# Performance work log

Measured on AMD Instinct MI355X. Metric: run time of the kernel, lower is better.

The kernel has to match this reference:

```python
import jax, jax.numpy as jnp
import numpy as np
from jax import lax

# 2D MPS-RNN (one-site, hilbert_local=2, real params, snake order, 'regular' phase)
# Faithful reconstruction of MPS_RNN_2D forward: site-by-site recurrence over an
# L x M lattice. At each site: candidate hidden states for both local occupations
#   h_cand[s] = M_h[i,j,s] @ h_left + M_v[i,j,s] @ h_below + v[i,j,s]
# conditional prob p(s) ~ sum_d eta[i,j,d]^2 * h_cand[s,d]^2 (eta-weighted norm),
# selected hidden state is renormalized; phase accumulates arg(w.h + c) (0 or pi
# for real params). Returns [B,2]: (log|psi|, phase).

L, M, S, D = 8, 8, 2, 32   # rows, cols, local Hilbert dim, bond dim dcut
B = 32768                  # batch of sampled configurations
NQ = L * M                 # nqubits
EPS = 1e-10


def setup_inputs() -> dict:
    key = jax.random.key(0)
    ks = jax.random.split(key, 7)
    sc = np.float32(1.0 / np.sqrt(D))  # keep hidden-state norms O(1)
    x = jax.random.randint(ks[0], (B, NQ), 0, 2, dtype=jnp.int32)
    M_h = jax.random.normal(ks[1], (L, M, S, D, D), jnp.float32) * sc
    M_v = jax.random.normal(ks[2], (L, M, S, D, D), jnp.float32) * sc
    v = jax.random.normal(ks[3], (L, M, S, D), jnp.float32) * sc
    w = jax.random.normal(ks[4], (L, M, D), jnp.float32) * sc
    c = jnp.zeros((L, M), jnp.float32)
    eta = jax.random.normal(ks[5], (L, M, D), jnp.float32)
    return {"x": x, "M_h": M_h, "M_v": M_v, "v": v, "w": w, "c": c, "eta": eta}


def _forward(x, M_h, M_v, v, w, c, eta):
    dt = M_h.dtype
    # snake order: odd rows are scanned right-to-left in lattice coordinates.
    cols = jnp.arange(M)
    odd = (jnp.arange(L) % 2 == 1)[:, None]
    colmap = jnp.where(odd, M - 1 - cols[None, :], cols[None, :])  # [L,M] scan-pos -> lattice col (involution)
    ri = jnp.arange(L)[:, None]
    gather = lambda p: p[ri, colmap]  # reorder params into scan order per row
    M_h_s, M_v_s, v_s, w_s, c_s, eta_s = (gather(p) for p in (M_h, M_v, v, w, c, eta))
    x_s = x.reshape(B, L, M).transpose(1, 2, 0)  # [L,M,B] already in qubit/scan order

    pi_f = jnp.asarray(np.pi, dt)

    def col_step(h_h, cin):
        Mh, Mv, vv, ww, cc, ee, xx, hv = cin
        # candidate states for both local occupations: [B,S,D]
        hc = (jnp.einsum('sab,Bb->Bsa', Mh, h_h)
              + jnp.einsum('sab,Bb->Bsa', Mv, hv)
              + vv[None])
        p = jnp.einsum('Bsa,a->Bs', hc * hc, ee * ee)  # eta-weighted squared norms
        psel = jnp.take_along_axis(p, xx[:, None], axis=1)[:, 0]
        dla = 0.5 * (jnp.log(psel + EPS) - jnp.log(p.sum(-1) + EPS))
        hsel = jnp.take_along_axis(hc, xx[:, None, None], axis=1)[:, 0]  # [B,D]
        hn = hsel / (jnp.sqrt(jnp.sum(hsel * hsel, -1, keepdims=True)) + EPS)
        a = hn @ ww + cc  # [B]
        dph = jnp.where(a < 0, pi_f, jnp.asarray(0, dt))  # arg of real scalar
        return hn, (dla, dph, hn)

    def row_step(carry, rin):
        h_v_lat, la, ph = carry
        Mh_r, Mv_r, v_r, w_r, c_r, e_r, x_r, cmap = rin
        hv_scan = h_v_lat[:, cmap].transpose(1, 0, 2)  # [M,B,D] vertical inputs in scan order
        h0 = jnp.ones((B, D), dt)  # left_boundary = ones
        _, (dlas, dphs, hs) = lax.scan(col_step, h0, (Mh_r, Mv_r, v_r, w_r, c_r, e_r, x_r, hv_scan))
        la = la + dlas.sum(0)
        ph = ph + dphs.sum(0)
        h_new = hs.transpose(1, 0, 2)[:, cmap]  # back to lattice column order (cmap is an involution)
        return (h_new, la, ph), None

    init = (jnp.zeros((B, M, D), dt),  # bottom_boundary = zeros
            jnp.zeros((B,), dt), jnp.zeros((B,), dt))
    (hv, log_amp, phase), _ = lax.scan(row_step, init, (M_h_s, M_v_s, v_s, w_s, c_s, eta_s, x_s, colmap))
    return jnp.stack([log_amp, phase], axis=-1)  # [B,2]


def reference(x, M_h, M_v, v, w, c, eta):
    return _forward(x, M_h, M_v, v, w, c, eta)
```

## Files before the change

kernel.cpp:

```cpp
#include <hip/hip_runtime.h>

#define LROWS 8
#define MCOLS 8
#define BD 32
#define NSITE 64
#define SPB 64
#define BTOT 32768
#define NBLK (BTOT / SPB)
#define EPS 1e-10
#define PI_D 3.14159265358979323846

#define W_OFF 0
#define CB_OFF 262144
#define CC_OFF (262144 + 12288)
#define WS_DBLS (CC_OFF + 64)

__global__ void precompute_kernel(const float* __restrict__ M_h,
                                  const float* __restrict__ M_v,
                                  const float* __restrict__ v,
                                  const float* __restrict__ w,
                                  const float* __restrict__ cc,
                                  const float* __restrict__ eta,
                                  double* __restrict__ ws) {
    int idx = blockIdx.x * 256 + threadIdx.x;
    if (idx >= WS_DBLS) return;
    double val = 0.0;
    if (idx < CB_OFF) {
        int pair = idx & 1, a8 = (idx >> 1) & 7, b = (idx >> 4) & 31;
        int r = (idx >> 9) & 7, site = idx >> 12;
        int i = site >> 3, js = site & 7;
        int c = (i & 1) ? (MCOLS - 1 - js) : js;
        int s = r >> 2, a = (r & 3) * 8 + a8;
        if (pair == 0) val = (double)M_h[(((i * MCOLS + c) * 2 + s) * BD + a) * BD + b];
        else           val = (double)M_v[(((i * MCOLS + c) * 2 + s) * BD + a) * BD + b];
    } else if (idx < CC_OFF) {
        int j = idx - CB_OFF;
        int site = j / 192;
        int rem = j - site * 192;
        int r = rem / 24, t = rem - r * 24;
        int i = site >> 3, js = site & 7;
        int c = (i & 1) ? (MCOLS - 1 - js) : js;
        int s = r >> 2, a0 = (r & 3) * 8;
        if (t < 8)       val = (double)v[(((i * MCOLS + c) * 2 + s) * BD) + a0 + t];
        else if (t < 16) { double e = (double)eta[(i * MCOLS + c) * BD + a0 + (t - 8)]; val = e * e; }
        else             val = (double)w[(i * MCOLS + c) * BD + a0 + (t - 16)];
    } else {
        int site = idx - CC_OFF;
        int i = site >> 3, js = site & 7;
        int c = (i & 1) ? (MCOLS - 1 - js) : js;
        val = (double)cc[i * MCOLS + c];
    }
    ws[idx] = val;
}

__launch_bounds__(512, 2)
__global__ void mps_main_kernel(const int* __restrict__ x,
                                const double* __restrict__ ws,
                                float* __restrict__ out) {
    __shared__ double hRow[MCOLS][BD][SPB];
    __shared__ double hOnes[BD][SPB];
    __shared__ double pbuf[8][SPB];
    __shared__ double ssb[8][SPB];
    __shared__ double phb[8][SPB];

    const int tid = threadIdx.x;
    const int k = tid & 63;
    const int r = tid >> 6;
    const int r_u = __builtin_amdgcn_readfirstlane(r);
    const int s = r_u >> 2;
    const int abase = (r_u & 3) * 8;
    const long kg = (long)blockIdx.x * SPB + k;

    for (int t = tid; t < MCOLS * BD * SPB; t += 512) (&hRow[0][0][0])[t] = 0.0;
    for (int t = tid; t < BD * SPB; t += 512) (&hOnes[0][0])[t] = 1.0;
    __syncthreads();

    const double2* __restrict__ Wp = (const double2*)ws;

    double la = 0.0, ph = 0.0;
    double2 wreg[2][16];

    {
        const double2* __restrict__ w0 = Wp + (size_t)(0 * 8 + r_u) * 256;
        #pragma unroll
        for (int t = 0; t < 16; ++t) wreg[0][t] = w0[t];
    }

    for (int i = 0; i < LROWS; ++i) {
        const int* xp = x + kg * NSITE + i * MCOLS;
        int4 xa = *reinterpret_cast<const int4*>(xp);
        int4 xb = *reinterpret_cast<const int4*>(xp + 4);
        const unsigned xbits = (unsigned)((xa.x & 1)        | ((xa.y & 1) << 1) |
                                          ((xa.z & 1) << 2) | ((xa.w & 1) << 3) |
                                          ((xb.x & 1) << 4) | ((xb.y & 1) << 5) |
                                          ((xb.z & 1) << 6) | ((xb.w & 1) << 7));
        double prodN = 1.0, prodD = 1.0;

        for (int js = 0; js < MCOLS; ++js) {
            const int site = i * MCOLS + js;
            const int c = (i & 1) ? (MCOLS - 1 - js) : js;
            const int cprev = (i & 1) ? (MCOLS - js) : (js - 1);

            const double2* __restrict__ wsite = Wp + (size_t)(site * 8 + r_u) * 256;
            const double*  __restrict__ cb    = ws + CB_OFF + (size_t)(site * 8 + r_u) * 24;

            const double* __restrict__ colV = &hRow[c][0][0];
            const double* __restrict__ colL = (js == 0) ? &hOnes[0][0] : &hRow[cprev][0][0];

            double acc[8];
            #pragma unroll
            for (int a = 0; a < 8; ++a) acc[a] = 0.0;

            #pragma unroll
            for (int bb = 0; bb < 16; ++bb) {
                const int cur = bb & 1;
                if (bb < 15) {
                    const double2* __restrict__ wn = wsite + (bb + 1) * 16;
                    #pragma unroll
                    for (int t = 0; t < 16; ++t) wreg[cur ^ 1][t] = wn[t];
                }
                #pragma unroll
                for (int bq = 0; bq < 2; ++bq) {
                    const int b = bb * 2 + bq;
                    const double hlb = colL[b * SPB + k];
                    const double hvb = colV[b * SPB + k];
                    #pragma unroll
                    for (int a = 0; a < 8; ++a) {
                        const double2 w2 = wreg[cur][bq * 8 + a];
                        acc[a] = fma(w2.x, hlb, fma(w2.y, hvb, acc[a]));
                    }
                }
            }
            #pragma unroll
            for (int a = 0; a < 8; ++a) acc[a] += cb[a];

            double pp = 0.0, ssp = 0.0, php = 0.0;
            #pragma unroll
            for (int a = 0; a < 8; ++a) {
                const double t2 = acc[a] * acc[a];
                pp  = fma(t2, cb[8 + a], pp);
                ssp += t2;
                php = fma(acc[a], cb[16 + a], php);
            }
            const double ccoef = ws[CC_OFF + site];
            const int xs = (int)((xbits >> js) & 1u);
            const bool sel = (s == xs);

            pbuf[r][k] = pp;
            ssb[r][k]  = ssp;
            phb[r][k]  = php;
            __syncthreads();

            {
                const double2* __restrict__ wn = Wp + (size_t)((site + 1) * 8 + r_u) * 256;
                #pragma unroll
                for (int t = 0; t < 16; ++t) wreg[0][t] = wn[t];
            }

            const double p0 = ((pbuf[0][k] + pbuf[1][k]) + pbuf[2][k]) + pbuf[3][k];
            const double p1 = ((pbuf[4][k] + pbuf[5][k]) + pbuf[6][k]) + pbuf[7][k];
            const double psel = xs ? p1 : p0;
            prodN *= (psel + EPS);
            prodD *= (p0 + p1 + EPS);

            const int gb = xs * 4;
            const double ss = ((ssb[gb][k] + ssb[gb + 1][k]) + ssb[gb + 2][k]) + ssb[gb + 3][k];
            const double inv = 1.0 / (sqrt(ss) + EPS);
            if (sel) {
                #pragma unroll
                for (int a = 0; a < 8; ++a)
                    hRow[c][abase + a][k] = acc[a] * inv;
            }
            const double phd = ((phb[gb][k] + phb[gb + 1][k]) + phb[gb + 2][k]) + phb[gb + 3][k];
            const double aph = phd * inv + ccoef;
            ph += (aph < 0.0) ? PI_D : 0.0;

            __syncthreads();
        }
        la += 0.5 * (log(prodN) - log(prodD));
    }

    if (r == 0) {
        out[kg * 2]     = (float)la;
        out[kg * 2 + 1] = (float)ph;
    }
}

extern "C" void kernel_launch(void* const* d_in, const int* in_sizes, int n_in,
                              void* d_out, int out_size, void* d_ws, size_t ws_size,
                              hipStream_t stream) {
    const int*   x    = (const int*)d_in[0];
    const float* M_h  = (const float*)d_in[1];
    const float* M_v  = (const float*)d_in[2];
    const float* v    = (const float*)d_in[3];
    const float* w    = (const float*)d_in[4];
    const float* cc   = (const float*)d_in[5];
    const float* eta  = (const float*)d_in[6];
    float* out = (float*)d_out;
    double* ws = (double*)d_ws;

    const int pre_total = WS_DBLS;
    dim3 preGrid((pre_total + 255) / 256), preBlock(256);
    hipLaunchKernelGGL(precompute_kernel, preGrid, preBlock, 0, stream,
                       M_h, M_v, v, w, cc, eta, ws);

    dim3 grid(NBLK), block(512);
    hipLaunchKernelGGL(mps_main_kernel, grid, block, 0, stream, x, ws, out);
}
```

Baseline: 707.7 us.

## Defer hidden-state normalization and fold left-boundary ones into bias

Stores unnormalized hidden states and applies the per-sample 1/||h|| scale as a scalar multiplier on the horizontal and vertical accumulations, so the normalization no longer waits on the reduction before the write. The js==0 left boundary of ones is folded into the bias during precompute, so the first column skips the horizontal matvec and the hOnes buffer. Reduction buffers are double-buffered by parity, and the next site's weight prefetch is merged into the main loop. The barrier count per site stays at two, and the separate H and V accumulators raise register pressure.

```diff
diff --git a/kernel.cpp b/kernel.cpp
--- a/kernel.cpp
+++ b/kernel.cpp
@@ -41,7 +41,15 @@
         int i = site >> 3, js = site & 7;
         int c = (i & 1) ? (MCOLS - 1 - js) : js;
         int s = r >> 2, a0 = (r & 3) * 8;
-        if (t < 8)       val = (double)v[(((i * MCOLS + c) * 2 + s) * BD) + a0 + t];
+        if (t < 8) {
+            val = (double)v[(((i * MCOLS + c) * 2 + s) * BD) + a0 + t];
+            if (js == 0) {
+                double sum = 0.0;
+                for (int b = 0; b < BD; ++b)
+                    sum += (double)M_h[(((i * MCOLS + c) * 2 + s) * BD + (a0 + t)) * BD + b];
+                val += sum;
+            }
+        }
         else if (t < 16) { double e = (double)eta[(i * MCOLS + c) * BD + a0 + (t - 8)]; val = e * e; }
         else             val = (double)w[(i * MCOLS + c) * BD + a0 + (t - 16)];
     } else {
@@ -58,10 +66,10 @@
                                 const double* __restrict__ ws,
                                 float* __restrict__ out) {
     __shared__ double hRow[MCOLS][BD][SPB];
-    __shared__ double hOnes[BD][SPB];
-    __shared__ double pbuf[8][SPB];
-    __shared__ double ssb[8][SPB];
-    __shared__ double phb[8][SPB];
+    __shared__ double invRow[MCOLS][SPB];
+    __shared__ double pbuf[2][8][SPB];
+    __shared__ double ssb[2][8][SPB];
+    __shared__ double phb[2][8][SPB];
 
     const int tid = threadIdx.x;
     const int k = tid & 63;
@@ -72,16 +80,18 @@
     const long kg = (long)blockIdx.x * SPB + k;
 
     for (int t = tid; t < MCOLS * BD * SPB; t += 512) (&hRow[0][0][0])[t] = 0.0;
-    for (int t = tid; t < BD * SPB; t += 512) (&hOnes[0][0])[t] = 1.0;
+    for (int t = tid; t < MCOLS * SPB; t += 512) (&invRow[0][0])[t] = 1.0;
     __syncthreads();
 
     const double2* __restrict__ Wp = (const double2*)ws;
 
     double la = 0.0, ph = 0.0;
+    double inv_l = 1.0;
+    int par = 0;
     double2 wreg[2][16];
 
     {
-        const double2* __restrict__ w0 = Wp + (size_t)(0 * 8 + r_u) * 256;
+        const double2* __restrict__ w0 = Wp + (size_t)r_u * 256;
         #pragma unroll
         for (int t = 0; t < 16; ++t) wreg[0][t] = w0[t];
     }
@@ -105,34 +115,64 @@
             const double*  __restrict__ cb    = ws + CB_OFF + (size_t)(site * 8 + r_u) * 24;
 
             const double* __restrict__ colV = &hRow[c][0][0];
-            const double* __restrict__ colL = (js == 0) ? &hOnes[0][0] : &hRow[cprev][0][0];
-
-            double acc[8];
+            const double* __restrict__ colL = &hRow[(js == 0) ? 0 : cprev][0][0];
+
+            const double invB = invRow[c][k];
+
+            double accH[8], accV[8];
             #pragma unroll
-            for (int a = 0; a < 8; ++a) acc[a] = 0.0;
-
-            #pragma unroll
-            for (int bb = 0; bb < 16; ++bb) {
-                const int cur = bb & 1;
-                if (bb < 15) {
-                    const double2* __restrict__ wn = wsite + (bb + 1) * 16;
+            for (int a = 0; a < 8; ++a) { accH[a] = 0.0; accV[a] = 0.0; }
+
+            if (js == 0) {
+                #pragma unroll
+                for (int bb = 0; bb < 16; ++bb) {
+                    const int cur = bb & 1;
+                    const double2* __restrict__ wn =
+                        (bb < 15) ? (wsite + (bb + 1) * 16) : (wsite + 2048);
                     #pragma unroll
                     for (int t = 0; t < 16; ++t) wreg[cur ^ 1][t] = wn[t];
-                }
-                #pragma unroll
-                for (int bq = 0; bq < 2; ++bq) {
-                    const int b = bb * 2 + bq;
-                    const double hlb = colL[b * SPB + k];
-                    const double hvb = colV[b * SPB + k];
-                    #pragma unroll
-                    for (int a = 0; a < 8; ++a) {
-                        const double2 w2 = wreg[cur][bq * 8 + a];
-                        acc[a] = fma(w2.x, hlb, fma(w2.y, hvb, acc[a]));
+                    #pragma unroll
+                    for (int bq = 0; bq < 2; ++bq) {
+                        const int b = bb * 2 + bq;
+                        const double hvb = colV[b * SPB + k];
+                        #pragma unroll
+                        for (int a = 0; a < 8; ++a)
+                            accV[a] = fma(wreg[cur][bq * 8 + a].y, hvb, accV[a]);
                     }
                 }
-            }
-            #pragma unroll
-            for (int a = 0; a < 8; ++a) acc[a] += cb[a];
+            } else {
+                #pragma unroll
+                for (int bb = 0; bb < 16; ++bb) {
+                    const int cur = bb & 1;
+                    const double2* __restrict__ wn =
+                        (bb < 15) ? (wsite + (bb + 1) * 16) : (wsite + 2048);
+                    #pragma unroll
+                    for (int t = 0; t < 16; ++t) wreg[cur ^ 1][t] = wn[t];
+                    #pragma unroll
+                    for (int bq = 0; bq < 2; ++bq) {
+                        const int b = bb * 2 + bq;
+                        const double hlb = colL[b * SPB + k];
+                        const double hvb = colV[b * SPB + k];
+                        #pragma unroll
+                        for (int a = 0; a < 8; ++a) {
+                            const double2 w2 = wreg[cur][bq * 8 + a];
+                            accH[a] = fma(w2.x, hlb, accH[a]);
+                            accV[a] = fma(w2.y, hvb, accV[a]);
+                        }
+                    }
+                }
+            }
+
+            double acc[8];
+            if (js == 0) {
+                #pragma unroll
+                for (int a = 0; a < 8; ++a)
+                    acc[a] = fma(accV[a], invB, cb[a]);
+            } else {
+                #pragma unroll
+                for (int a = 0; a < 8; ++a)
+                    acc[a] = fma(accH[a], inv_l, fma(accV[a], invB, cb[a]));
+            }
 
             double pp = 0.0, ssp = 0.0, php = 0.0;
             #pragma unroll
@@ -146,36 +186,35 @@
             const int xs = (int)((xbits >> js) & 1u);
             const bool sel = (s == xs);
 
-            pbuf[r][k] = pp;
-            ssb[r][k]  = ssp;
-            phb[r][k]  = php;
+            pbuf[par][r][k] = pp;
+            ssb[par][r][k]  = ssp;
+            phb[par][r][k]  = php;
             __syncthreads();
 
-            {
-                const double2* __restrict__ wn = Wp + (size_t)((site + 1) * 8 + r_u) * 256;
-                #pragma unroll
-                for (int t = 0; t < 16; ++t) wreg[0][t] = wn[t];
-            }
-
-            const double p0 = ((pbuf[0][k] + pbuf[1][k]) + pbuf[2][k]) + pbuf[3][k];
-            const double p1 = ((pbuf[4][k] + pbuf[5][k]) + pbuf[6][k]) + pbuf[7][k];
+            if (sel) {
+                #pragma unroll
+                for (int a = 0; a < 8; ++a)
+                    hRow[c][abase + a][k] = acc[a];
+            }
+            __syncthreads();
+
+            const double p0 = ((pbuf[par][0][k] + pbuf[par][1][k]) + pbuf[par][2][k]) + pbuf[par][3][k];
+            const double p1 = ((pbuf[par][4][k] + pbuf[par][5][k]) + pbuf[par][6][k]) + pbuf[par][7][k];
             const double psel = xs ? p1 : p0;
             prodN *= (psel + EPS);
             prodD *= (p0 + p1 + EPS);
 
             const int gb = xs * 4;
-            const double ss = ((ssb[gb][k] + ssb[gb + 1][k]) + ssb[gb + 2][k]) + ssb[gb + 3][k];
+            const double ss = ((ssb[par][gb][k] + ssb[par][gb + 1][k]) + ssb[par][gb + 2][k]) + ssb[par][gb + 3][k];
             const double inv = 1.0 / (sqrt(ss) + EPS);
-            if (sel) {
-                #pragma unroll
-                for (int a = 0; a < 8; ++a)
-                    hRow[c][abase + a][k] = acc[a] * inv;
-            }
-            const double phd = ((phb[gb][k] + phb[gb + 1][k]) + phb[gb + 2][k]) + phb[gb + 3][k];
+            inv_l = inv;
+            if (r == 0) invRow[c][k] = inv;
+
+            const double phd = ((phb[par][gb][k] + phb[par][gb + 1][k]) + phb[par][gb + 2][k]) + phb[par][gb + 3][k];
             const double aph = phd * inv + ccoef;
             ph += (aph < 0.0) ? PI_D : 0.0;
 
-            __syncthreads();
+            par ^= 1;
         }
         la += 0.5 * (log(prodN) - log(prodD));
     }
```

Result: slower. 1.430 ms (+102.1%).

## Split per-site work across 16 waves with 4 outputs each, drop ones buffer

Applied to the files above, without the earlier changes.

Each block now runs 1024 threads (16 waves), and each wave computes 4 hidden-state rows instead of 8, so per-thread accumulators and weight registers are halved. The precompute kernel re-packs weights and per-row coefficients to match the new 16-row partition. The left-boundary ones buffer is removed: the first column gets a specialized loop that adds the weight directly. Probability and phase reductions are now done only by wave 0. This trades more waves per block and larger cross-wave reductions for lower register pressure and shorter serial FMA chains per thread, while occupancy drops to one block per CU.

```diff
diff --git a/kernel.cpp b/kernel.cpp
--- a/kernel.cpp
+++ b/kernel.cpp
@@ -26,24 +26,24 @@
     if (idx >= WS_DBLS) return;
     double val = 0.0;
     if (idx < CB_OFF) {
-        int pair = idx & 1, a8 = (idx >> 1) & 7, b = (idx >> 4) & 31;
-        int r = (idx >> 9) & 7, site = idx >> 12;
+        int pair = idx & 1, a4 = (idx >> 1) & 3, b = (idx >> 3) & 31;
+        int r = (idx >> 8) & 15, site = idx >> 12;
         int i = site >> 3, js = site & 7;
         int c = (i & 1) ? (MCOLS - 1 - js) : js;
-        int s = r >> 2, a = (r & 3) * 8 + a8;
+        int s = r >> 3, a = (r & 7) * 4 + a4;
         if (pair == 0) val = (double)M_h[(((i * MCOLS + c) * 2 + s) * BD + a) * BD + b];
         else           val = (double)M_v[(((i * MCOLS + c) * 2 + s) * BD + a) * BD + b];
     } else if (idx < CC_OFF) {
         int j = idx - CB_OFF;
         int site = j / 192;
         int rem = j - site * 192;
-        int r = rem / 24, t = rem - r * 24;
+        int r = rem / 12, t = rem - r * 12;
         int i = site >> 3, js = site & 7;
         int c = (i & 1) ? (MCOLS - 1 - js) : js;
-        int s = r >> 2, a0 = (r & 3) * 8;
-        if (t < 8)       val = (double)v[(((i * MCOLS + c) * 2 + s) * BD) + a0 + t];
-        else if (t < 16) { double e = (double)eta[(i * MCOLS + c) * BD + a0 + (t - 8)]; val = e * e; }
-        else             val = (double)w[(i * MCOLS + c) * BD + a0 + (t - 16)];
+        int s = r >> 3, a0 = (r & 7) * 4;
+        if (t < 4)      val = (double)v[(((i * MCOLS + c) * 2 + s) * BD) + a0 + t];
+        else if (t < 8) { double e = (double)eta[(i * MCOLS + c) * BD + a0 + (t - 4)]; val = e * e; }
+        else            val = (double)w[(i * MCOLS + c) * BD + a0 + (t - 8)];
     } else {
         int site = idx - CC_OFF;
         int i = site >> 3, js = site & 7;
@@ -53,37 +53,36 @@
     ws[idx] = val;
 }
 
-__launch_bounds__(512, 2)
+__launch_bounds__(1024, 1)
 __global__ void mps_main_kernel(const int* __restrict__ x,
                                 const double* __restrict__ ws,
                                 float* __restrict__ out) {
     __shared__ double hRow[MCOLS][BD][SPB];
-    __shared__ double hOnes[BD][SPB];
-    __shared__ double pbuf[8][SPB];
-    __shared__ double ssb[8][SPB];
-    __shared__ double phb[8][SPB];
+    __shared__ double pbuf[16][SPB];
+    __shared__ double ssb[16][SPB];
+    __shared__ double phb[16][SPB];
 
     const int tid = threadIdx.x;
     const int k = tid & 63;
     const int r = tid >> 6;
     const int r_u = __builtin_amdgcn_readfirstlane(r);
-    const int s = r_u >> 2;
-    const int abase = (r_u & 3) * 8;
+    const int s = r_u >> 3;
+    const int abase = (r_u & 7) * 4;
     const long kg = (long)blockIdx.x * SPB + k;
 
-    for (int t = tid; t < MCOLS * BD * SPB; t += 512) (&hRow[0][0][0])[t] = 0.0;
-    for (int t = tid; t < BD * SPB; t += 512) (&hOnes[0][0])[t] = 1.0;
+    for (int t = tid; t < MCOLS * BD * SPB; t += 1024) (&hRow[0][0][0])[t] = 0.0;
     __syncthreads();
 
     const double2* __restrict__ Wp = (const double2*)ws;
 
     double la = 0.0, ph = 0.0;
-    double2 wreg[2][16];
+    double prodN = 1.0, prodD = 1.0;
+    double2 wreg[2][8];
 
     {
-        const double2* __restrict__ w0 = Wp + (size_t)(0 * 8 + r_u) * 256;
+        const double2* __restrict__ w0 = Wp + (size_t)r_u * 128;
         #pragma unroll
-        for (int t = 0; t < 16; ++t) wreg[0][t] = w0[t];
+        for (int t = 0; t < 8; ++t) wreg[0][t] = w0[t];
     }
 
     for (int i = 0; i < LROWS; ++i) {
@@ -94,53 +93,75 @@
                                           ((xa.z & 1) << 2) | ((xa.w & 1) << 3) |
                                           ((xb.x & 1) << 4) | ((xb.y & 1) << 5) |
                                           ((xb.z & 1) << 6) | ((xb.w & 1) << 7));
-        double prodN = 1.0, prodD = 1.0;
+        prodN = 1.0; prodD = 1.0;
 
         for (int js = 0; js < MCOLS; ++js) {
             const int site = i * MCOLS + js;
             const int c = (i & 1) ? (MCOLS - 1 - js) : js;
             const int cprev = (i & 1) ? (MCOLS - js) : (js - 1);
 
-            const double2* __restrict__ wsite = Wp + (size_t)(site * 8 + r_u) * 256;
-            const double*  __restrict__ cb    = ws + CB_OFF + (size_t)(site * 8 + r_u) * 24;
+            const double2* __restrict__ wsite = Wp + (size_t)(site * 16 + r_u) * 128;
+            const double*  __restrict__ cb    = ws + CB_OFF + (size_t)(site * 16 + r_u) * 12;
 
             const double* __restrict__ colV = &hRow[c][0][0];
-            const double* __restrict__ colL = (js == 0) ? &hOnes[0][0] : &hRow[cprev][0][0];
-
-            double acc[8];
+
+            double acc[4];
             #pragma unroll
-            for (int a = 0; a < 8; ++a) acc[a] = 0.0;
-
+            for (int a = 0; a < 4; ++a) acc[a] = 0.0;
+
+            if (js == 0) {
+                #pragma unroll
+                for (int bb = 0; bb < 16; ++bb) {
+                    const int cur = bb & 1;
+                    if (bb < 15) {
+                        const double2* __restrict__ wn = wsite + (bb + 1) * 8;
+                        #pragma unroll
+                        for (int t = 0; t < 8; ++t) wreg[cur ^ 1][t] = wn[t];
+                    }
+                    #pragma unroll
+                    for (int bq = 0; bq < 2; ++bq) {
+                        const int b = bb * 2 + bq;
+                        const double hvb = colV[b * SPB + k];
+                        #pragma unroll
+                        for (int a = 0; a < 4; ++a) {
+                            const double2 w2 = wreg[cur][bq * 4 + a];
+                            acc[a] = fma(w2.y, hvb, acc[a] + w2.x);
+                        }
+                    }
+                }
+            } else {
+                const double* __restrict__ colL = &hRow[cprev][0][0];
+                #pragma unroll
+                for (int bb = 0; bb < 16; ++bb) {
+                    const int cur = bb & 1;
+                    if (bb < 15) {
+                        const double2* __restrict__ wn = wsite + (bb + 1) * 8;
+                        #pragma unroll
+                        for (int t = 0; t < 8; ++t) wreg[cur ^ 1][t] = wn[t];
+                    }
+                    #pragma unroll
+                    for (int bq = 0; bq < 2; ++bq) {
+                        const int b = bb * 2 + bq;
+                        const double hlb = colL[b * SPB + k];
+                        const double hvb = colV[b * SPB + k];
+                        #pragma unroll
+                        for (int a = 0; a < 4; ++a) {
+                            const double2 w2 = wreg[cur][bq * 4 + a];
+                            acc[a] = fma(w2.x, hlb, fma(w2.y, hvb, acc[a]));
+                        }
+                    }
+                }
+            }
             #pragma unroll
-            for (int bb = 0; bb < 16; ++bb) {
-                const int cur = bb & 1;
-                if (bb < 15) {
-                    const double2* __restrict__ wn = wsite + (bb + 1) * 16;
-                    #pragma unroll
-                    for (int t = 0; t < 16; ++t) wreg[cur ^ 1][t] = wn[t];
-                }
-                #pragma unroll
-                for (int bq = 0; bq < 2; ++bq) {
-                    const int b = bb * 2 + bq;
-                    const double hlb = colL[b * SPB + k];
-                    const double hvb = colV[b * SPB + k];
-                    #pragma unroll
-                    for (int a = 0; a < 8; ++a) {
-                        const double2 w2 = wreg[cur][bq * 8 + a];
-                        acc[a] = fma(w2.x, hlb, fma(w2.y, hvb, acc[a]));
-                    }
-                }
-            }
-            #pragma unroll
-            for (int a = 0; a < 8; ++a) acc[a] += cb[a];
+            for (int a = 0; a < 4; ++a) acc[a] += cb[a];
 
             double pp = 0.0, ssp = 0.0, php = 0.0;
             #pragma unroll
-            for (int a = 0; a < 8; ++a) {
+            for (int a = 0; a < 4; ++a) {
                 const double t2 = acc[a] * acc[a];
-                pp  = fma(t2, cb[8 + a], pp);
+                pp  = fma(t2, cb[4 + a], pp);
                 ssp += t2;
-                php = fma(acc[a], cb[16 + a], php);
+                php = fma(acc[a], cb[8 + a], php);
             }
             const double ccoef = ws[CC_OFF + site];
             const int xs = (int)((xbits >> js) & 1u);
@@ -152,32 +173,38 @@
             __syncthreads();
 
             {
-                const double2* __restrict__ wn = Wp + (size_t)((site + 1) * 8 + r_u) * 256;
-                #pragma unroll
-                for (int t = 0; t < 16; ++t) wreg[0][t] = wn[t];
-            }
-
-            const double p0 = ((pbuf[0][k] + pbuf[1][k]) + pbuf[2][k]) + pbuf[3][k];
-            const double p1 = ((pbuf[4][k] + pbuf[5][k]) + pbuf[6][k]) + pbuf[7][k];
-            const double psel = xs ? p1 : p0;
-            prodN *= (psel + EPS);
-            prodD *= (p0 + p1 + EPS);
-
-            const int gb = xs * 4;
-            const double ss = ((ssb[gb][k] + ssb[gb + 1][k]) + ssb[gb + 2][k]) + ssb[gb + 3][k];
+                const double2* __restrict__ wn = Wp + (size_t)((site + 1) * 16 + r_u) * 128;
+                #pragma unroll
+                for (int t = 0; t < 8; ++t) wreg[0][t] = wn[t];
+            }
+
+            const int gb = xs * 8;
+            const double ss = (((ssb[gb][k] + ssb[gb + 1][k]) + (ssb[gb + 2][k] + ssb[gb + 3][k]))
+                             + ((ssb[gb + 4][k] + ssb[gb + 5][k]) + (ssb[gb + 6][k] + ssb[gb + 7][k])));
             const double inv = 1.0 / (sqrt(ss) + EPS);
             if (sel) {
                 #pragma unroll
-                for (int a = 0; a < 8; ++a)
+                for (int a = 0; a < 4; ++a)
                     hRow[c][abase + a][k] = acc[a] * inv;
             }
-            const double phd = ((phb[gb][k] + phb[gb + 1][k]) + phb[gb + 2][k]) + phb[gb + 3][k];
-            const double aph = phd * inv + ccoef;
-            ph += (aph < 0.0) ? PI_D : 0.0;
+
+            if (r_u == 0) {
+                const double p0 = (((pbuf[0][k] + pbuf[1][k]) + (pbuf[2][k] + pbuf[3][k]))
+                                 + ((pbuf[4][k] + pbuf[5][k]) + (pbuf[6][k] + pbuf[7][k])));
+                const double p1 = (((pbuf[8][k] + pbuf[9][k]) + (pbuf[10][k] + pbuf[11][k]))
+                                 + ((pbuf[12][k] + pbuf[13][k]) + (pbuf[14][k] + pbuf[15][k])));
+                const double psel = xs ? p1 : p0;
+                prodN *= (psel + EPS);
+                prodD *= (p0 + p1 + EPS);
+                const double phd = (((phb[gb][k] + phb[gb + 1][k]) + (phb[gb + 2][k] + phb[gb + 3][k]))
+                                  + ((phb[gb + 4][k] + phb[gb + 5][k]) + (phb[gb + 6][k] + phb[gb + 7][k])));
+                const double aph = phd * inv + ccoef;
+                ph += (aph < 0.0) ? PI_D : 0.0;
+            }
 
             __syncthreads();
         }
-        la += 0.5 * (log(prodN) - log(prodD));
+        if (r_u == 0) la += 0.5 * (log(prodN) - log(prodD));
     }
 
     if (r == 0) {
@@ -204,6 +231,6 @@
     hipLaunchKernelGGL(precompute_kernel, preGrid, preBlock, 0, stream,
                        M_h, M_v, v, w, cc, eta, ws);
 
-    dim3 grid(NBLK), block(512);
+    dim3 grid(NBLK), block(1024);
     hipLaunchKernelGGL(mps_main_kernel, grid, block, 0, stream, x, ws, out);
 }
```

New measurement: 663.3 us. 6.3% less time.

## Use 4 waves per block with 16 outputs per wave and contiguous weight stream

Applied to the files above, without the earlier changes.

Each block now has 4 waves of 64 lanes instead of 8. Each wave computes 16 hidden outputs instead of 8, which halves how often each h value is read from LDS per output. Weights are relaid out so each wave reads one contiguous per-wave stream across all sites, with a 4-deep rotating register prefetch. The left-boundary ones buffer is replaced by a special path that adds the weight directly. Only wave 0 now does the probability and phase reductions. The trade-off is fewer waves per block and more registers per thread, which may reduce occupancy and the ability to hide latency.

```diff
diff --git a/kernel.cpp b/kernel.cpp
--- a/kernel.cpp
+++ b/kernel.cpp
@@ -26,24 +26,24 @@
     if (idx >= WS_DBLS) return;
     double val = 0.0;
     if (idx < CB_OFF) {
-        int pair = idx & 1, a8 = (idx >> 1) & 7, b = (idx >> 4) & 31;
-        int r = (idx >> 9) & 7, site = idx >> 12;
+        int pair = idx & 1, a16 = (idx >> 1) & 15, b = (idx >> 5) & 31;
+        int site = (idx >> 10) & 63, r = idx >> 16;
         int i = site >> 3, js = site & 7;
         int c = (i & 1) ? (MCOLS - 1 - js) : js;
-        int s = r >> 2, a = (r & 3) * 8 + a8;
+        int s = r >> 1, a = (r & 1) * 16 + a16;
         if (pair == 0) val = (double)M_h[(((i * MCOLS + c) * 2 + s) * BD + a) * BD + b];
         else           val = (double)M_v[(((i * MCOLS + c) * 2 + s) * BD + a) * BD + b];
     } else if (idx < CC_OFF) {
         int j = idx - CB_OFF;
         int site = j / 192;
         int rem = j - site * 192;
-        int r = rem / 24, t = rem - r * 24;
+        int r = rem / 48, t = rem - r * 48;
         int i = site >> 3, js = site & 7;
         int c = (i & 1) ? (MCOLS - 1 - js) : js;
-        int s = r >> 2, a0 = (r & 3) * 8;
-        if (t < 8)       val = (double)v[(((i * MCOLS + c) * 2 + s) * BD) + a0 + t];
-        else if (t < 16) { double e = (double)eta[(i * MCOLS + c) * BD + a0 + (t - 8)]; val = e * e; }
-        else             val = (double)w[(i * MCOLS + c) * BD + a0 + (t - 16)];
+        int s = r >> 1, a0 = (r & 1) * 16;
+        if (t < 16)      val = (double)v[(((i * MCOLS + c) * 2 + s) * BD) + a0 + t];
+        else if (t < 32) { double e = (double)eta[(i * MCOLS + c) * BD + a0 + (t - 16)]; val = e * e; }
+        else             val = (double)w[(i * MCOLS + c) * BD + a0 + (t - 32)];
     } else {
         int site = idx - CC_OFF;
         int i = site >> 3, js = site & 7;
@@ -53,37 +53,37 @@
     ws[idx] = val;
 }
 
-__launch_bounds__(512, 2)
+__launch_bounds__(256, 1)
 __global__ void mps_main_kernel(const int* __restrict__ x,
                                 const double* __restrict__ ws,
                                 float* __restrict__ out) {
     __shared__ double hRow[MCOLS][BD][SPB];
-    __shared__ double hOnes[BD][SPB];
-    __shared__ double pbuf[8][SPB];
-    __shared__ double ssb[8][SPB];
-    __shared__ double phb[8][SPB];
+    __shared__ double pbuf[4][SPB];
+    __shared__ double ssb[4][SPB];
+    __shared__ double phb[4][SPB];
 
     const int tid = threadIdx.x;
     const int k = tid & 63;
     const int r = tid >> 6;
     const int r_u = __builtin_amdgcn_readfirstlane(r);
-    const int s = r_u >> 2;
-    const int abase = (r_u & 3) * 8;
+    const int s = r_u >> 1;
+    const int abase = (r_u & 1) * 16;
     const long kg = (long)blockIdx.x * SPB + k;
 
-    for (int t = tid; t < MCOLS * BD * SPB; t += 512) (&hRow[0][0][0])[t] = 0.0;
-    for (int t = tid; t < BD * SPB; t += 512) (&hOnes[0][0])[t] = 1.0;
+    for (int t = tid; t < MCOLS * BD * SPB; t += 256) (&hRow[0][0][0])[t] = 0.0;
     __syncthreads();
 
     const double2* __restrict__ Wp = (const double2*)ws;
+    const double2* __restrict__ wstream0 = Wp + (size_t)r_u * (NSITE * 512);
 
     double la = 0.0, ph = 0.0;
-    double2 wreg[2][16];
+    double2 wreg[4][8];
 
     {
-        const double2* __restrict__ w0 = Wp + (size_t)(0 * 8 + r_u) * 256;
         #pragma unroll
-        for (int t = 0; t < 16; ++t) wreg[0][t] = w0[t];
+        for (int cch = 0; cch < 4; ++cch)
+            #pragma unroll
+            for (int t = 0; t < 8; ++t) wreg[cch][t] = wstream0[cch * 8 + t];
     }
 
     for (int i = 0; i < LROWS; ++i) {
@@ -101,46 +101,62 @@
             const int c = (i & 1) ? (MCOLS - 1 - js) : js;
             const int cprev = (i & 1) ? (MCOLS - js) : (js - 1);
 
-            const double2* __restrict__ wsite = Wp + (size_t)(site * 8 + r_u) * 256;
-            const double*  __restrict__ cb    = ws + CB_OFF + (size_t)(site * 8 + r_u) * 24;
+            const double2* __restrict__ wsite = wstream0 + (size_t)site * 512;
+            const double*  __restrict__ cb    = ws + CB_OFF + (size_t)(site * 4 + r_u) * 48;
 
             const double* __restrict__ colV = &hRow[c][0][0];
-            const double* __restrict__ colL = (js == 0) ? &hOnes[0][0] : &hRow[cprev][0][0];
-
-            double acc[8];
-            #pragma unroll
-            for (int a = 0; a < 8; ++a) acc[a] = 0.0;
-
-            #pragma unroll
-            for (int bb = 0; bb < 16; ++bb) {
-                const int cur = bb & 1;
-                if (bb < 15) {
-                    const double2* __restrict__ wn = wsite + (bb + 1) * 16;
+
+            double acc[16];
+            #pragma unroll
+            for (int a = 0; a < 16; ++a) acc[a] = 0.0;
+
+            if (js == 0) {
+                #pragma unroll
+                for (int b = 0; b < BD; ++b) {
+                    const double hvb = colV[b * SPB + k];
                     #pragma unroll
-                    for (int t = 0; t < 16; ++t) wreg[cur ^ 1][t] = wn[t];
+                    for (int hf = 0; hf < 2; ++hf) {
+                        const int ch = 2 * b + hf;
+                        #pragma unroll
+                        for (int t = 0; t < 8; ++t) {
+                            const double2 w2 = wreg[ch & 3][t];
+                            acc[hf * 8 + t] = fma(w2.y, hvb, acc[hf * 8 + t] + w2.x);
+                        }
+                        const double2* __restrict__ wn = wsite + (ch + 4) * 8;
+                        #pragma unroll
+                        for (int t = 0; t < 8; ++t) wreg[ch & 3][t] = wn[t];
+                    }
                 }
+            } else {
+                const double* __restrict__ colL = &hRow[cprev][0][0];
                 #pragma unroll
-                for (int bq = 0; bq < 2; ++bq) {
-                    const int b = bb * 2 + bq;
+                for (int b = 0; b < BD; ++b) {
                     const double hlb = colL[b * SPB + k];
                     const double hvb = colV[b * SPB + k];
                     #pragma unroll
-                    for (int a = 0; a < 8; ++a) {
-                        const double2 w2 = wreg[cur][bq * 8 + a];
-                        acc[a] = fma(w2.x, hlb, fma(w2.y, hvb, acc[a]));
+                    for (int hf = 0; hf < 2; ++hf) {
+                        const int ch = 2 * b + hf;
+                        #pragma unroll
+                        for (int t = 0; t < 8; ++t) {
+                            const double2 w2 = wreg[ch & 3][t];
+                            acc[hf * 8 + t] = fma(w2.x, hlb, fma(w2.y, hvb, acc[hf * 8 + t]));
+                        }
+                        const double2* __restrict__ wn = wsite + (ch + 4) * 8;
+                        #pragma unroll
+                        for (int t = 0; t < 8; ++t) wreg[ch & 3][t] = wn[t];
                     }
                 }
             }
             #pragma unroll
-            for (int a = 0; a < 8; ++a) acc[a] += cb[a];
+            for (int a = 0; a < 16; ++a) acc[a] += cb[a];
 
             double pp = 0.0, ssp = 0.0, php = 0.0;
             #pragma unroll
-            for (int a = 0; a < 8; ++a) {
+            for (int a = 0; a < 16; ++a) {
                 const double t2 = acc[a] * acc[a];
-                pp  = fma(t2, cb[8 + a], pp);
+                pp  = fma(t2, cb[16 + a], pp);
                 ssp += t2;
-                php = fma(acc[a], cb[16 + a], php);
+                php = fma(acc[a], cb[32 + a], php);
             }
             const double ccoef = ws[CC_OFF + site];
             const int xs = (int)((xbits >> js) & 1u);
@@ -151,33 +167,29 @@
             phb[r][k]  = php;
             __syncthreads();
 
-            {
-                const double2* __restrict__ wn = Wp + (size_t)((site + 1) * 8 + r_u) * 256;
-                #pragma unroll
-                for (int t = 0; t < 16; ++t) wreg[0][t] = wn[t];
-            }
-
-            const double p0 = ((pbuf[0][k] + pbuf[1][k]) + pbuf[2][k]) + pbuf[3][k];
-            const double p1 = ((pbuf[4][k] + pbuf[5][k]) + pbuf[6][k]) + pbuf[7][k];
-            const double psel = xs ? p1 : p0;
-            prodN *= (psel + EPS);
-            prodD *= (p0 + p1 + EPS);
-
-            const int gb = xs * 4;
-            const double ss = ((ssb[gb][k] + ssb[gb + 1][k]) + ssb[gb + 2][k]) + ssb[gb + 3][k];
+            const int gb = xs * 2;
+            const double ss = ssb[gb][k] + ssb[gb + 1][k];
             const double inv = 1.0 / (sqrt(ss) + EPS);
             if (sel) {
                 #pragma unroll
-                for (int a = 0; a < 8; ++a)
+                for (int a = 0; a < 16; ++a)
                     hRow[c][abase + a][k] = acc[a] * inv;
             }
-            const double phd = ((phb[gb][k] + phb[gb + 1][k]) + phb[gb + 2][k]) + phb[gb + 3][k];
-            const double aph = phd * inv + ccoef;
-            ph += (aph < 0.0) ? PI_D : 0.0;
+
+            if (r_u == 0) {
+                const double p0 = pbuf[0][k] + pbuf[1][k];
+                const double p1 = pbuf[2][k] + pbuf[3][k];
+                const double psel = xs ? p1 : p0;
+                prodN *= (psel + EPS);
+                prodD *= (p0 + p1 + EPS);
+                const double phd = phb[gb][k] + phb[gb + 1][k];
+                const double aph = phd * inv + ccoef;
+                ph += (aph < 0.0) ? PI_D : 0.0;
+            }
 
             __syncthreads();
         }
-        la += 0.5 * (log(prodN) - log(prodD));
+        if (r_u == 0) la += 0.5 * (log(prodN) - log(prodD));
     }
 
     if (r == 0) {
@@ -204,6 +216,6 @@
     hipLaunchKernelGGL(precompute_kernel, preGrid, preBlock, 0, stream,
                        M_h, M_v, v, w, cc, eta, ws);
 
-    dim3 grid(NBLK), block(512);
+    dim3 grid(NBLK), block(256);
     hipLaunchKernelGGL(mps_main_kernel, grid, block, 0, stream, x, ws, out);
 }
```

New measurement: 2.009 ms. 184% more time.
